# Optimization experiments

Measured on AMD Instinct MI355X. Metric: run time of the kernel, lower is better.

Reference implementation:

```python
import jax, jax.numpy as jnp
import numpy as np

VOCAB = 50257
N_EMBD = 640
BLOCK = 256
B = 16


def setup_inputs() -> dict:
    key = jax.random.key(0)
    ks = jax.random.split(key, 8)
    std = 0.02
    return {
        "idx": jax.random.randint(ks[0], (B, BLOCK), 0, VOCAB, dtype=jnp.int64 if jax.config.jax_enable_x64 else jnp.int32),
        "w_embed": jax.random.normal(ks[1], (VOCAB, N_EMBD), jnp.float32) * std,
        "w_pos": jax.random.normal(ks[2], (BLOCK, N_EMBD), jnp.float32) * std,
        "wq": jax.random.normal(ks[3], (N_EMBD, N_EMBD), jnp.float32) * std,
        "wk": jax.random.normal(ks[4], (N_EMBD, N_EMBD), jnp.float32) * std,
        "wv": jax.random.normal(ks[5], (N_EMBD, N_EMBD), jnp.float32) * std,
        "w_out": jax.random.normal(ks[6], (VOCAB, N_EMBD), jnp.float32) * std,
        "b_out": jnp.zeros((VOCAB,), jnp.float32),
    }


def reference(idx, w_embed, w_pos, wq, wk, wv, w_out, b_out):
    # idx: (B, T) token ids. Dropout is identity (eval mode).
    Bt, T = idx.shape
    x = w_embed[idx] + w_pos[:T]                      # (B, T, D)
    q = jnp.einsum('btd,ed->bte', x, wq)              # torch Linear: x @ W.T
    k = jnp.einsum('btd,ed->bte', x, wk)
    v = jnp.einsum('btd,ed->bte', x, wv)
    scale = jnp.asarray(N_EMBD ** 0.5, x.dtype)
    scores = jnp.einsum('btd,bsd->bts', q, k) / scale  # (B, T, T)
    causal = jnp.triu(jnp.ones((T, T), bool), k=1)     # True above diagonal
    scores = jnp.where(causal, jnp.asarray(-jnp.inf, scores.dtype), scores)
    attn = jax.nn.softmax(scores, axis=-1)
    attn_out = jnp.einsum('bts,bsd->btd', attn, v)     # (B, T, D)
    logits = jnp.einsum('btd,vd->btv', attn_out, w_out) + b_out  # (B, T, V)
    return logits
```

## Files before the change

kernel.cpp:

```cpp
#include <hip/hip_runtime.h>
#include <hip/hip_bf16.h>
#include <stdint.h>

#define VOCAB 50257
#define VPAD  50432
#define DIM   640
#define SEQ   256
#define NBATCH 16
#define MROWS 4096

using bf16 = __hip_bfloat16;
typedef __attribute__((ext_vector_type(8))) short short8;
typedef __attribute__((ext_vector_type(4))) float f32x4;
struct bf16x4 { bf16 a, b, c, d; };

__device__ __forceinline__ void gld_lds16(const void* g, void* l) {
  __builtin_amdgcn_global_load_lds(
      (const __attribute__((address_space(1))) void*)g,
      (__attribute__((address_space(3))) void*)l, 16, 0, 0);
}

#define BAR() asm volatile("s_barrier" ::: "memory")
#define VMC0() asm volatile("s_waitcnt vmcnt(0)" ::: "memory")

__global__ void embed_kernel(const int* __restrict__ idx,
                             const float* __restrict__ we,
                             const float* __restrict__ wp,
                             bf16* __restrict__ xb) {
  int row = blockIdx.x;
  int t = row & (SEQ - 1);
  int tok = idx[row];
  const float* src = we + (long)tok * DIM;
  const float* pos = wp + (long)t * DIM;
  for (int d = threadIdx.x * 4; d < DIM; d += blockDim.x * 4) {
    float4 s = *(const float4*)(src + d);
    float4 p = *(const float4*)(pos + d);
    bf16x4 o = { __float2bfloat16(s.x + p.x), __float2bfloat16(s.y + p.y),
                 __float2bfloat16(s.z + p.z), __float2bfloat16(s.w + p.w) };
    *(bf16x4*)(xb + (long)row * DIM + d) = o;
  }
}

__global__ void conv4_kernel(const float* __restrict__ src, bf16* __restrict__ dst,
                             long n_src, long n_dst) {
  long i = ((long)blockIdx.x * blockDim.x + threadIdx.x) * 4;
  long stride = (long)gridDim.x * blockDim.x * 4;
  for (; i < n_dst; i += stride) {
    float4 v = (i < n_src) ? *(const float4*)(src + i) : make_float4(0.f, 0.f, 0.f, 0.f);
    bf16x4 o = { __float2bfloat16(v.x), __float2bfloat16(v.y),
                 __float2bfloat16(v.z), __float2bfloat16(v.w) };
    *(bf16x4*)(dst + i) = o;
  }
}

__global__ void softmax_kernel(const float* __restrict__ sc, bf16* __restrict__ p) {
  int wid = threadIdx.x >> 6, lane = threadIdx.x & 63;
  int row = blockIdx.x * 4 + wid;
  int t = row & (SEQ - 1);
  const float* srow = sc + (long)row * SEQ;
  const float rsc = 0.03952847075210474f;
  float v[4];
  float mx = -1e30f;
#pragma unroll
  for (int i = 0; i < 4; ++i) {
    int s = lane + 64 * i;
    v[i] = (s <= t) ? srow[s] * rsc : -1e30f;
    mx = fmaxf(mx, v[i]);
  }
#pragma unroll
  for (int off = 32; off; off >>= 1) mx = fmaxf(mx, __shfl_xor(mx, off, 64));
  float sum = 0.f;
#pragma unroll
  for (int i = 0; i < 4; ++i) {
    int s = lane + 64 * i;
    v[i] = (s <= t) ? __expf(v[i] - mx) : 0.f;
    sum += v[i];
  }
#pragma unroll
  for (int off = 32; off; off >>= 1) sum += __shfl_xor(sum, off, 64);
  float inv = 1.f / sum;
#pragma unroll
  for (int i = 0; i < 4; ++i)
    p[(long)row * SEQ + lane + 64 * i] = __float2bfloat16(v[i] * inv);
}

template <int NT, typename OUT_T, bool BIAS, bool TRV>
__global__ __launch_bounds__(256, 4) void gemm_pipe(
    const bf16* __restrict__ Ag, const bf16* __restrict__ Bg,
    OUT_T* __restrict__ Cg, const float* __restrict__ bias,
    int K, int ldc, int Nstore, long sA, long sB, long sC) {
  __shared__ __align__(16) char lds[32768];
  const int tid = threadIdx.x;
  const int lane = tid & 63, wv = tid >> 6;
  const int lr = lane & 15, h16 = lane >> 4;

  const int tm = blockIdx.x, tn = blockIdx.y, bz = blockIdx.z;
  const bf16* A = Ag + (long)bz * sA + (long)tm * 128 * K;
  const bf16* B = Bg + (long)bz * sB + (long)tn * 128 * K;

  int srcE[2], dstW[2];
#pragma unroll
  for (int j = 0; j < 2; ++j) {
    int d = j * 256 + tid;
    int b = d ^ ((d >> 3) & 3);
    srcE[j] = (b >> 2) * K + (b & 3) * 8;
    dstW[j] = (j * 256 + wv * 64) * 16;
  }
  const bf16* aS0 = A + srcE[0];
  const bf16* aS1 = A + srcE[1];
  const bf16* bS0 = B + srcE[0];
  const bf16* bS1 = B + srcE[1];
  auto STAGE = [&](int slot, int t) {
    int kOff = t * 32;
    gld_lds16(aS0 + kOff, lds + slot + dstW[0]);
    gld_lds16(aS1 + kOff, lds + slot + dstW[1]);
    gld_lds16(bS0 + kOff, lds + slot + 8192 + dstW[0]);
    gld_lds16(bS1 + kOff, lds + slot + 8192 + dstW[1]);
  };

  const int wr = (wv >> 1) * 64, wc = (wv & 1) * 64;
  int aoff[4], boff[4];
#pragma unroll
  for (int m = 0; m < 4; ++m) {
    int La = (wr + m * 16 + lr) * 64 + h16 * 16;
    aoff[m] = La ^ (((La >> 7) & 3) << 4);
    int Lb = (wc + m * 16 + lr) * 64 + h16 * 16;
    boff[m] = 8192 + (Lb ^ (((Lb >> 7) & 3) << 4));
  }

  f32x4 acc[4][4] = {};
  short8 a[4], b[4];

  STAGE(0, 0);
  VMC0();
  BAR();

#pragma unroll 2
  for (int t = 0; t < NT; ++t) {
    const int cur = (t & 1) * 16384;
    if (t + 1 < NT) STAGE(16384 - cur, t + 1);
#pragma unroll
    for (int m = 0; m < 4; ++m) a[m] = *(const short8*)(lds + cur + aoff[m]);
#pragma unroll
    for (int n = 0; n < 4; ++n) b[n] = *(const short8*)(lds + cur + boff[n]);
    __builtin_amdgcn_s_setprio(1);
#pragma unroll
    for (int m = 0; m < 4; ++m)
#pragma unroll
      for (int n = 0; n < 4; ++n)
        acc[m][n] = __builtin_amdgcn_mfma_f32_16x16x32_bf16(a[m], b[n], acc[m][n], 0, 0, 0);
    __builtin_amdgcn_s_setprio(0);
    if (t + 1 < NT) VMC0();
    BAR();
  }

  if constexpr (sizeof(OUT_T) == 4) {
    float* Cf = (float*)Cg + (long)bz * sC;
    float bv[4];
#pragma unroll
    for (int n = 0; n < 4; ++n) {
      int col = tn * 128 + wc + lr + n * 16;
      bv[n] = (BIAS && col < Nstore) ? bias[col] : 0.f;
    }
    char* reg = lds + wv * 8192;
    const int rowL = lane & 31, cb = lane >> 5;
#pragma unroll
    for (int mm = 0; mm < 2; ++mm) {
#pragma unroll
      for (int mp = 0; mp < 2; ++mp)
#pragma unroll
        for (int n = 0; n < 4; ++n) {
          f32x4 v = acc[mm * 2 + mp][n];
          v[0] += bv[n]; v[1] += bv[n]; v[2] += bv[n]; v[3] += bv[n];
          int col = lr + n * 16;
          int rho = mp * 16 + h16 * 4;
          int w = col * 32 + (rho ^ ((col & 7) << 2));
          *(f32x4*)(reg + w * 4) = v;
        }
      const long rowg = tm * 128 + wr + mm * 32 + rowL;
#pragma unroll
      for (int k = 0; k < 8; ++k) {
        f32x4 o;
#pragma unroll
        for (int c = 0; c < 4; ++c) {
          int col = k * 8 + cb * 4 + c;
          int w = col * 32 + (rowL ^ ((col & 7) << 2));
          o[c] = *(const float*)(reg + w * 4);
        }
        int gcol = tn * 128 + wc + k * 8 + cb * 4;
        float* dst = Cf + rowg * (long)ldc + gcol;
        if (gcol + 3 < Nstore) {
          *(f32x4*)dst = o;
        } else {
#pragma unroll
          for (int c = 0; c < 4; ++c)
            if (gcol + c < Nstore) dst[c] = o[c];
        }
      }
    }
  } else {
    OUT_T* C = Cg + (long)bz * sC;
    const int crow0 = tm * 128 + wr + h16 * 4;
    const int ccol0 = tn * 128 + wc + lr;
#pragma unroll
    for (int m = 0; m < 4; ++m)
#pragma unroll
      for (int n = 0; n < 4; ++n) {
        int col = ccol0 + n * 16;
        if (col < Nstore) {
#pragma unroll
          for (int j = 0; j < 4; ++j) {
            long row = crow0 + m * 16 + j;
            if constexpr (TRV) {
              C[((long)(row >> 8) * DIM + col) * SEQ + (row & 255)] =
                  __float2bfloat16(acc[m][n][j]);
            } else {
              C[row * ldc + col] = __float2bfloat16(acc[m][n][j]);
            }
          }
        }
      }
  }
}

__global__ __launch_bounds__(256, 6) void scores64(
    const bf16* __restrict__ qg, const bf16* __restrict__ kg,
    float* __restrict__ sc) {
  const int tm = blockIdx.x, tn = blockIdx.y, bz = blockIdx.z;
  if (tn > tm) return;
  __shared__ __align__(16) char lds[16384];
  const int tid = threadIdx.x;
  const int lane = tid & 63, wv = tid >> 6;
  const int lr = lane & 15, h16 = lane >> 4;

  const bf16* A = qg + (long)bz * SEQ * DIM + (long)tm * 64 * DIM;
  const bf16* B = kg + (long)bz * SEQ * DIM + (long)tn * 64 * DIM;

  int srcE, dstW;
  {
    int d = tid;
    int b = d ^ ((d >> 3) & 3);
    srcE = (b >> 2) * DIM + (b & 3) * 8;
    dstW = (wv * 64) * 16;
  }
  auto STAGE = [&](int slot, int t) {
    int kOff = t * 32;
    gld_lds16(A + srcE + kOff, lds + slot + dstW);
    gld_lds16(B + srcE + kOff, lds + slot + 4096 + dstW);
  };

  const int wm = wv >> 1, wn = wv & 1;
  int aoff[2], boff[2];
#pragma unroll
  for (int m = 0; m < 2; ++m) {
    int La = (wm * 32 + m * 16 + lr) * 64 + h16 * 16;
    aoff[m] = La ^ (((La >> 7) & 3) << 4);
    int Lb = (wn * 32 + m * 16 + lr) * 64 + h16 * 16;
    boff[m] = 4096 + (Lb ^ (((Lb >> 7) & 3) << 4));
  }

  f32x4 acc[2][2] = {};
  short8 a[2], b[2];

  STAGE(0, 0);
  VMC0();
  BAR();

#pragma unroll 2
  for (int t = 0; t < 20; ++t) {
    const int cur = (t & 1) * 8192;
    if (t + 1 < 20) STAGE(8192 - cur, t + 1);
#pragma unroll
    for (int m = 0; m < 2; ++m) a[m] = *(const short8*)(lds + cur + aoff[m]);
#pragma unroll
    for (int n = 0; n < 2; ++n) b[n] = *(const short8*)(lds + cur + boff[n]);
    __builtin_amdgcn_s_setprio(1);
#pragma unroll
    for (int m = 0; m < 2; ++m)
#pragma unroll
      for (int n = 0; n < 2; ++n)
        acc[m][n] = __builtin_amdgcn_mfma_f32_16x16x32_bf16(a[m], b[n], acc[m][n], 0, 0, 0);
    __builtin_amdgcn_s_setprio(0);
    if (t + 1 < 20) VMC0();
    BAR();
  }

  float* S = sc + (long)bz * SEQ * SEQ;
  const int crow0 = tm * 64 + wm * 32 + h16 * 4;
  const int ccol0 = tn * 64 + wn * 32 + lr;
#pragma unroll
  for (int m = 0; m < 2; ++m)
#pragma unroll
    for (int n = 0; n < 2; ++n)
#pragma unroll
      for (int j = 0; j < 4; ++j)
        S[(long)(crow0 + m * 16 + j) * SEQ + ccol0 + n * 16] = acc[m][n][j];
}

__global__ __launch_bounds__(512, 6) void gemm8(
    const bf16* __restrict__ Ag, const bf16* __restrict__ Bg,
    float* __restrict__ Cg, const float* __restrict__ bias) {
  __shared__ __align__(16) char lds[32768];
  const int tid = threadIdx.x;
  const int lane = tid & 63, wv = tid >> 6;
  const int lr = lane & 15, h16 = lane >> 4;

  const int tm = blockIdx.x, tn = blockIdx.y;
  const bf16* A = Ag + (long)tm * 128 * DIM;
  const bf16* B = Bg + (long)tn * 128 * DIM;

  int srcE, dstW;
  {
    int d = tid;
    int b = d ^ ((d >> 3) & 3);
    srcE = (b >> 2) * DIM + (b & 3) * 8;
    dstW = (wv * 64) * 16;
  }
  const bf16* aS = A + srcE;
  const bf16* bS = B + srcE;
  auto STAGE = [&](int slot, int t) {
    int kOff = t * 32;
    gld_lds16(aS + kOff, lds + slot + dstW);
    gld_lds16(bS + kOff, lds + slot + 8192 + dstW);
  };

  const int wr = (wv >> 2) * 64, wc = (wv & 3) * 32;
  int aoff[4], boff[2];
#pragma unroll
  for (int m = 0; m < 4; ++m) {
    int La = (wr + m * 16 + lr) * 64 + h16 * 16;
    aoff[m] = La ^ (((La >> 7) & 3) << 4);
  }
#pragma unroll
  for (int n = 0; n < 2; ++n) {
    int Lb = (wc + n * 16 + lr) * 64 + h16 * 16;
    boff[n] = 8192 + (Lb ^ (((Lb >> 7) & 3) << 4));
  }

  f32x4 acc[4][2] = {};
  short8 a[4], b[2];

  STAGE(0, 0);
  VMC0();
  BAR();

#pragma unroll 2
  for (int t = 0; t < 20; ++t) {
    const int cur = (t & 1) * 16384;
    if (t + 1 < 20) STAGE(16384 - cur, t + 1);
#pragma unroll
    for (int m = 0; m < 4; ++m) a[m] = *(const short8*)(lds + cur + aoff[m]);
#pragma unroll
    for (int n = 0; n < 2; ++n) b[n] = *(const short8*)(lds + cur + boff[n]);
    __builtin_amdgcn_s_setprio(1);
#pragma unroll
    for (int m = 0; m < 4; ++m)
#pragma unroll
      for (int n = 0; n < 2; ++n)
        acc[m][n] = __builtin_amdgcn_mfma_f32_16x16x32_bf16(a[m], b[n], acc[m][n], 0, 0, 0);
    __builtin_amdgcn_s_setprio(0);
    if (t + 1 < 20) VMC0();
    BAR();
  }

  const int crow0 = tm * 128 + wr + h16 * 4;
  const int ccol0 = tn * 128 + wc + lr;
  float bv[2];
#pragma unroll
  for (int n = 0; n < 2; ++n) {
    int col = ccol0 + n * 16;
    bv[n] = (col < VOCAB) ? bias[col] : 0.f;
  }
#pragma unroll
  for (int m = 0; m < 4; ++m)
#pragma unroll
    for (int n = 0; n < 2; ++n) {
      int col = ccol0 + n * 16;
      if (col < VOCAB) {
#pragma unroll
        for (int j = 0; j < 4; ++j)
          Cg[(long)(crow0 + m * 16 + j) * VOCAB + col] = acc[m][n][j] + bv[n];
      }
    }
}

extern "C" void kernel_launch(void* const* d_in, const int* in_sizes, int n_in,
                              void* d_out, int out_size, void* d_ws, size_t ws_size,
                              hipStream_t stream) {
  const int*   idx     = (const int*)d_in[0];
  const float* w_embed = (const float*)d_in[1];
  const float* w_pos   = (const float*)d_in[2];
  const float* wq      = (const float*)d_in[3];
  const float* wk      = (const float*)d_in[4];
  const float* wv      = (const float*)d_in[5];
  const float* w_out   = (const float*)d_in[6];
  const float* b_out   = (const float*)d_in[7];
  float* out = (float*)d_out;

  size_t off = 0;
  auto alloc = [&](size_t bytes) {
    void* p = (char*)d_ws + off;
    off += (bytes + 255) & ~(size_t)255;
    return p;
  };
  bf16* x_bf    = (bf16*)alloc((size_t)MROWS * DIM * 2);
  bf16* wqkv_bf = (bf16*)alloc((size_t)3 * DIM * DIM * 2);
  bf16* wout_bf = (bf16*)alloc((size_t)VPAD * DIM * 2);
  bf16* qkv     = (bf16*)alloc((size_t)2 * MROWS * DIM * 2);
  bf16* vT      = (bf16*)alloc((size_t)NBATCH * DIM * SEQ * 2);
  float* scores = (float*)alloc((size_t)NBATCH * SEQ * SEQ * 4);
  bf16* P       = (bf16*)alloc((size_t)NBATCH * SEQ * SEQ * 2);
  bf16* attn    = (bf16*)alloc((size_t)MROWS * DIM * 2);

  const long QKV_S = (long)MROWS * DIM;
  const long W_S   = (long)DIM * DIM;

  embed_kernel<<<MROWS, 256, 0, stream>>>(idx, w_embed, w_pos, x_bf);

  conv4_kernel<<<256, 256, 0, stream>>>(wq, wqkv_bf,           W_S, W_S);
  conv4_kernel<<<256, 256, 0, stream>>>(wk, wqkv_bf + W_S,     W_S, W_S);
  conv4_kernel<<<256, 256, 0, stream>>>(wv, wqkv_bf + 2 * W_S, W_S, W_S);
  conv4_kernel<<<2048, 256, 0, stream>>>(w_out, wout_bf, (long)VOCAB * DIM, (long)VPAD * DIM);

  gemm_pipe<20, bf16, false, false><<<dim3(MROWS / 128, DIM / 128, 2), 256, 0, stream>>>(
      x_bf, wqkv_bf, qkv, nullptr, DIM, DIM, DIM, 0, W_S, QKV_S);

  gemm_pipe<20, bf16, false, true><<<dim3(MROWS / 128, DIM / 128, 1), 256, 0, stream>>>(
      x_bf, wqkv_bf + 2 * W_S, vT, nullptr, DIM, DIM, DIM, 0, 0, 0);

  scores64<<<dim3(4, 4, NBATCH), 256, 0, stream>>>(qkv, qkv + QKV_S, scores);

  softmax_kernel<<<MROWS / 4, 256, 0, stream>>>(scores, P);

  gemm_pipe<8, bf16, false, false><<<dim3(SEQ / 128, DIM / 128, NBATCH), 256, 0, stream>>>(
      P, vT, attn, nullptr, SEQ, DIM, DIM,
      (long)SEQ * SEQ, (long)DIM * SEQ, (long)SEQ * DIM);

  gemm8<<<dim3(MROWS / 128, VPAD / 128), 512, 0, stream>>>(attn, wout_bf, out, b_out);
}
```

Before: 600.2 us.

## Fuse w_out fp32-to-bf16 conversion into output GEMM and merge QKV weight conversions

```diff
diff --git a/kernel.cpp b/kernel.cpp
--- a/kernel.cpp
+++ b/kernel.cpp
@@ -18,6 +18,11 @@
   __builtin_amdgcn_global_load_lds(
       (const __attribute__((address_space(1))) void*)g,
       (__attribute__((address_space(3))) void*)l, 16, 0, 0);
+}
+
+__device__ __forceinline__ short f2bs(float f) {
+  bf16 t = __float2bfloat16(f);
+  return *reinterpret_cast<short*>(&t);
 }
 
 #define BAR() asm volatile("s_barrier" ::: "memory")
@@ -41,15 +46,18 @@
   }
 }
 
-__global__ void conv4_kernel(const float* __restrict__ src, bf16* __restrict__ dst,
-                             long n_src, long n_dst) {
+__global__ void conv3_kernel(const float* __restrict__ s0, const float* __restrict__ s1,
+                             const float* __restrict__ s2, bf16* __restrict__ dst,
+                             long n_each) {
+  const float* src = (blockIdx.y == 0) ? s0 : (blockIdx.y == 1) ? s1 : s2;
+  bf16* d = dst + (long)blockIdx.y * n_each;
   long i = ((long)blockIdx.x * blockDim.x + threadIdx.x) * 4;
   long stride = (long)gridDim.x * blockDim.x * 4;
-  for (; i < n_dst; i += stride) {
-    float4 v = (i < n_src) ? *(const float4*)(src + i) : make_float4(0.f, 0.f, 0.f, 0.f);
+  for (; i < n_each; i += stride) {
+    float4 v = *(const float4*)(src + i);
     bf16x4 o = { __float2bfloat16(v.x), __float2bfloat16(v.y),
                  __float2bfloat16(v.z), __float2bfloat16(v.w) };
-    *(bf16x4*)(dst + i) = o;
+    *(bf16x4*)(d + i) = o;
   }
 }
 
@@ -297,35 +305,45 @@
         S[(long)(crow0 + m * 16 + j) * SEQ + ccol0 + n * 16] = acc[m][n][j];
 }
 
-__global__ __launch_bounds__(512, 6) void gemm8(
-    const bf16* __restrict__ Ag, const bf16* __restrict__ Bg,
+__global__ __launch_bounds__(512, 6) void gemm8f(
+    const bf16* __restrict__ Ag, const float* __restrict__ Wg,
     float* __restrict__ Cg, const float* __restrict__ bias) {
-  __shared__ __align__(16) char lds[32768];
+  __shared__ __align__(16) char lds[49152];
   const int tid = threadIdx.x;
   const int lane = tid & 63, wv = tid >> 6;
   const int lr = lane & 15, h16 = lane >> 4;
 
   const int tm = blockIdx.x, tn = blockIdx.y;
   const bf16* A = Ag + (long)tm * 128 * DIM;
-  const bf16* B = Bg + (long)tn * 128 * DIM;
-
-  int srcE, dstW;
+
+  const bf16* aS;
+  int dstA;
   {
     int d = tid;
     int b = d ^ ((d >> 3) & 3);
-    srcE = (b >> 2) * DIM + (b & 3) * 8;
-    dstW = (wv * 64) * 16;
-  }
-  const bf16* aS = A + srcE;
-  const bf16* bS = B + srcE;
+    aS = A + (b >> 2) * DIM + (b & 3) * 8;
+    dstA = (wv * 64) * 16;
+  }
+  const float* bS[2];
+  int dstB[2];
+#pragma unroll
+  for (int j = 0; j < 2; ++j) {
+    int d = j * 512 + tid;
+    int b = d ^ ((d >> 3) & 7);
+    int grow = tn * 128 + (b >> 3);
+    if (grow > VOCAB - 1) grow = VOCAB - 1;
+    bS[j] = Wg + (long)grow * DIM + (b & 7) * 4;
+    dstB[j] = 8192 + (j * 512 + wv * 64) * 16;
+  }
   auto STAGE = [&](int slot, int t) {
-    int kOff = t * 32;
-    gld_lds16(aS + kOff, lds + slot + dstW);
-    gld_lds16(bS + kOff, lds + slot + 8192 + dstW);
+    gld_lds16(aS + t * 32, lds + slot + dstA);
+#pragma unroll
+    for (int j = 0; j < 2; ++j)
+      gld_lds16(bS[j] + t * 32, lds + slot + dstB[j]);
   };
 
   const int wr = (wv >> 2) * 64, wc = (wv & 3) * 32;
-  int aoff[4], boff[2];
+  int aoff[4], boff[2][2];
 #pragma unroll
   for (int m = 0; m < 4; ++m) {
     int La = (wr + m * 16 + lr) * 64 + h16 * 16;
@@ -333,8 +351,10 @@
   }
 #pragma unroll
   for (int n = 0; n < 2; ++n) {
-    int Lb = (wc + n * 16 + lr) * 64 + h16 * 16;
-    boff[n] = 8192 + (Lb ^ (((Lb >> 7) & 3) << 4));
+    int L = (wc + n * 16 + lr) * 128 + h16 * 32;
+    boff[n][0] = 8192 + (L ^ (((L >> 7) & 7) << 4));
+    int L1 = L + 16;
+    boff[n][1] = 8192 + (L1 ^ (((L1 >> 7) & 7) << 4));
   }
 
   f32x4 acc[4][2] = {};
@@ -346,12 +366,19 @@
 
 #pragma unroll 2
   for (int t = 0; t < 20; ++t) {
-    const int cur = (t & 1) * 16384;
-    if (t + 1 < 20) STAGE(16384 - cur, t + 1);
+    const int cur = (t & 1) * 24576;
+    if (t + 1 < 20) STAGE(24576 - cur, t + 1);
 #pragma unroll
     for (int m = 0; m < 4; ++m) a[m] = *(const short8*)(lds + cur + aoff[m]);
 #pragma unroll
-    for (int n = 0; n < 2; ++n) b[n] = *(const short8*)(lds + cur + boff[n]);
+    for (int n = 0; n < 2; ++n) {
+      f32x4 lo = *(const f32x4*)(lds + cur + boff[n][0]);
+      f32x4 hi = *(const f32x4*)(lds + cur + boff[n][1]);
+      short8 bb;
+      bb[0] = f2bs(lo[0]); bb[1] = f2bs(lo[1]); bb[2] = f2bs(lo[2]); bb[3] = f2bs(lo[3]);
+      bb[4] = f2bs(hi[0]); bb[5] = f2bs(hi[1]); bb[6] = f2bs(hi[2]); bb[7] = f2bs(hi[3]);
+      b[n] = bb;
+    }
     __builtin_amdgcn_s_setprio(1);
 #pragma unroll
     for (int m = 0; m < 4; ++m)
@@ -405,7 +432,6 @@
   };
   bf16* x_bf    = (bf16*)alloc((size_t)MROWS * DIM * 2);
   bf16* wqkv_bf = (bf16*)alloc((size_t)3 * DIM * DIM * 2);
-  bf16* wout_bf = (bf16*)alloc((size_t)VPAD * DIM * 2);
   bf16* qkv     = (bf16*)alloc((size_t)2 * MROWS * DIM * 2);
   bf16* vT      = (bf16*)alloc((size_t)NBATCH * DIM * SEQ * 2);
   float* scores = (float*)alloc((size_t)NBATCH * SEQ * SEQ * 4);
@@ -417,10 +443,7 @@
 
   embed_kernel<<<MROWS, 256, 0, stream>>>(idx, w_embed, w_pos, x_bf);
 
-  conv4_kernel<<<256, 256, 0, stream>>>(wq, wqkv_bf,           W_S, W_S);
-  conv4_kernel<<<256, 256, 0, stream>>>(wk, wqkv_bf + W_S,     W_S, W_S);
-  conv4_kernel<<<256, 256, 0, stream>>>(wv, wqkv_bf + 2 * W_S, W_S, W_S);
-  conv4_kernel<<<2048, 256, 0, stream>>>(w_out, wout_bf, (long)VOCAB * DIM, (long)VPAD * DIM);
+  conv3_kernel<<<dim3(256, 3), 256, 0, stream>>>(wq, wk, wv, wqkv_bf, W_S);
 
   gemm_pipe<20, bf16, false, false><<<dim3(MROWS / 128, DIM / 128, 2), 256, 0, stream>>>(
       x_bf, wqkv_bf, qkv, nullptr, DIM, DIM, DIM, 0, W_S, QKV_S);
@@ -436,5 +459,5 @@
       P, vT, attn, nullptr, SEQ, DIM, DIM,
       (long)SEQ * SEQ, (long)DIM * SEQ, (long)SEQ * DIM);
 
-  gemm8<<<dim3(MROWS / 128, VPAD / 128), 512, 0, stream>>>(attn, wout_bf, out, b_out);
-}
+  gemm8f<<<dim3(MROWS / 128, VPAD / 128), 512, 0, stream>>>(attn, w_out, out, b_out);
+}
```

After: 757.4 us. +26.2%, slower.

## Replace output GEMM with 256x256-tile persistent-column kernel and deeper pipelining

Applied to the files above, without the earlier changes.

```diff
diff --git a/kernel.cpp b/kernel.cpp
--- a/kernel.cpp
+++ b/kernel.cpp
@@ -3,7 +3,7 @@
 #include <stdint.h>
 
 #define VOCAB 50257
-#define VPAD  50432
+#define VPAD3 51200
 #define DIM   640
 #define SEQ   256
 #define NBATCH 16
@@ -21,6 +21,7 @@
 }
 
 #define BAR() asm volatile("s_barrier" ::: "memory")
+#define VMC(n) asm volatile("s_waitcnt vmcnt(" #n ")" ::: "memory")
 #define VMC0() asm volatile("s_waitcnt vmcnt(0)" ::: "memory")
 
 __global__ void embed_kernel(const int* __restrict__ idx,
@@ -297,91 +298,133 @@
         S[(long)(crow0 + m * 16 + j) * SEQ + ccol0 + n * 16] = acc[m][n][j];
 }
 
-__global__ __launch_bounds__(512, 6) void gemm8(
+__global__ __launch_bounds__(512, 1) void gemm256m(
     const bf16* __restrict__ Ag, const bf16* __restrict__ Bg,
     float* __restrict__ Cg, const float* __restrict__ bias) {
-  __shared__ __align__(16) char lds[32768];
+  __shared__ __align__(16) char lds[131072];
   const int tid = threadIdx.x;
   const int lane = tid & 63, wv = tid >> 6;
+  const int wm = wv >> 2, wn = wv & 3;
+  const int tm = blockIdx.x;
+  const int tg = blockIdx.y;
+
+  int e0, e1, du0, du1;
+  {
+    int L0 = tid * 16;
+    int L1 = (512 + tid) * 16;
+    int Lp0 = L0 ^ (((L0 >> 9) & 1) << 5);
+    int Lp1 = L1 ^ (((L1 >> 9) & 1) << 5);
+    e0 = ((Lp0 >> 6) & 127) * DIM + ((Lp0 >> 13) & 1) * 32 + ((Lp0 & 63) >> 1);
+    e1 = ((Lp1 >> 6) & 127) * DIM + ((Lp1 >> 13) & 1) * 32 + ((Lp1 & 63) >> 1);
+    du0 = (wv << 6) * 16;
+    du1 = (512 + (wv << 6)) * 16;
+  }
+  auto STAGE = [&](int halfBase, const bf16* src) {
+    gld_lds16(src + e0, lds + halfBase + du0);
+    gld_lds16(src + e1, lds + halfBase + du1);
+  };
+
+  const bf16* Ab = Ag + (long)tm * 256 * DIM;
+  const long STRIDE = (long)256 * DIM;
+
   const int lr = lane & 15, h16 = lane >> 4;
-
-  const int tm = blockIdx.x, tn = blockIdx.y;
-  const bf16* A = Ag + (long)tm * 128 * DIM;
-  const bf16* B = Bg + (long)tn * 128 * DIM;
-
-  int srcE, dstW;
-  {
-    int d = tid;
-    int b = d ^ ((d >> 3) & 3);
-    srcE = (b >> 2) * DIM + (b & 3) * 8;
-    dstW = (wv * 64) * 16;
-  }
-  const bf16* aS = A + srcE;
-  const bf16* bS = B + srcE;
-  auto STAGE = [&](int slot, int t) {
-    int kOff = t * 32;
-    gld_lds16(aS + kOff, lds + slot + dstW);
-    gld_lds16(bS + kOff, lds + slot + 8192 + dstW);
-  };
-
-  const int wr = (wv >> 2) * 64, wc = (wv & 3) * 32;
-  int aoff[4], boff[2];
-#pragma unroll
-  for (int m = 0; m < 4; ++m) {
-    int La = (wr + m * 16 + lr) * 64 + h16 * 16;
-    aoff[m] = La ^ (((La >> 7) & 3) << 4);
-  }
-#pragma unroll
-  for (int n = 0; n < 2; ++n) {
-    int Lb = (wc + n * 16 + lr) * 64 + h16 * 16;
-    boff[n] = 8192 + (Lb ^ (((Lb >> 7) & 3) << 4));
-  }
-
-  f32x4 acc[4][2] = {};
-  short8 a[4], b[2];
-
-  STAGE(0, 0);
-  VMC0();
+  const int laneOff = (lr * 64 + h16 * 16) ^ ((lr & 8) << 2);
+  const int abase = wm * 16384 + laneOff;
+  const int bbase = 32768 + (wn >> 1) * 16384 + (wn & 1) * 4096 + laneOff;
+
+  f32x4 acc[8][4] = {};
+  short8 a0[2][4], a1[2][4], b[2][4];
+
+#define READ_A(DST, SLOT, MFB)                                                \
+  { _Pragma("unroll") for (int ks = 0; ks < 2; ++ks)                          \
+    _Pragma("unroll") for (int mf = 0; mf < 4; ++mf)                          \
+      DST[ks][mf] = *(const short8*)(lds + (SLOT) + abase + ks * 8192 +       \
+                                     ((MFB) + mf) * 1024); }
+#define READ_B(SLOT)                                                          \
+  { _Pragma("unroll") for (int ks = 0; ks < 2; ++ks)                          \
+    _Pragma("unroll") for (int nf = 0; nf < 4; ++nf)                          \
+      b[ks][nf] = *(const short8*)(lds + (SLOT) + bbase + ks * 8192 +         \
+                                   nf * 1024); }
+#define MFMA_G(AARR, KS, ROFF)                                                \
+  __builtin_amdgcn_s_setprio(1);                                              \
+  { _Pragma("unroll") for (int mf = 0; mf < 4; ++mf)                          \
+    _Pragma("unroll") for (int nf = 0; nf < 4; ++nf)                          \
+      acc[(ROFF) + mf][nf] = __builtin_amdgcn_mfma_f32_16x16x32_bf16(         \
+          AARR[KS][mf], b[KS][nf], acc[(ROFF) + mf][nf], 0, 0, 0); }          \
+  __builtin_amdgcn_s_setprio(0);
+
+  const bf16* Bc = Bg + (long)tg * 4 * STRIDE;
+
+  STAGE(0,             Ab);
+  STAGE(16384,         Ab + 128 * DIM);
+  STAGE(32768,         Bc);
+  STAGE(49152,         Bc + 128 * DIM);
+  STAGE(65536 + 32768, Bc + 64);
+  STAGE(65536 + 0,     Ab + 64);
+  STAGE(65536 + 16384, Ab + 128 * DIM + 64);
+  VMC(6);
   BAR();
 
-#pragma unroll 2
-  for (int t = 0; t < 20; ++t) {
-    const int cur = (t & 1) * 16384;
-    if (t + 1 < 20) STAGE(16384 - cur, t + 1);
-#pragma unroll
-    for (int m = 0; m < 4; ++m) a[m] = *(const short8*)(lds + cur + aoff[m]);
-#pragma unroll
-    for (int n = 0; n < 2; ++n) b[n] = *(const short8*)(lds + cur + boff[n]);
-    __builtin_amdgcn_s_setprio(1);
-#pragma unroll
-    for (int m = 0; m < 4; ++m)
-#pragma unroll
-      for (int n = 0; n < 2; ++n)
-        acc[m][n] = __builtin_amdgcn_mfma_f32_16x16x32_bf16(a[m], b[n], acc[m][n], 0, 0, 0);
-    __builtin_amdgcn_s_setprio(0);
-    if (t + 1 < 20) VMC0();
-    BAR();
-  }
-
-  const int crow0 = tm * 128 + wr + h16 * 4;
-  const int ccol0 = tn * 128 + wc + lr;
-  float bv[2];
-#pragma unroll
-  for (int n = 0; n < 2; ++n) {
-    int col = ccol0 + n * 16;
-    bv[n] = (col < VOCAB) ? bias[col] : 0.f;
-  }
-#pragma unroll
-  for (int m = 0; m < 4; ++m)
-#pragma unroll
-    for (int n = 0; n < 2; ++n) {
-      int col = ccol0 + n * 16;
-      if (col < VOCAB) {
-#pragma unroll
-        for (int j = 0; j < 4; ++j)
-          Cg[(long)(crow0 + m * 16 + j) * VOCAB + col] = acc[m][n][j] + bv[n];
+  for (int s = 0; s < 4; ++s) {
+    const bf16* Bn = Bc + STRIDE;
+    const bool sNotLast = (s < 3);
+#pragma unroll
+    for (int T = 0; T < 10; ++T) {
+      const int slot = (T & 1) << 16;
+      const int nslot = ((T + 1) & 1) << 16;
+      const int k1 = (T < 9) ? (T + 1) * 64 : 0;
+      const int k2 = (T < 8) ? (T + 2) * 64 : (T - 8) * 64;
+      const bf16* B1src = (T < 9) ? Bc : Bn;
+      const bf16* B2src = (T < 8) ? Bc : Bn;
+      const bool ok1 = sNotLast || (T < 9);
+      const bool ok2 = sNotLast || (T < 8);
+      READ_A(a0, slot, 0);
+      READ_B(slot);
+      if (ok1) STAGE(nslot + 49152, B1src + 128 * DIM + k1);
+      BAR();
+      MFMA_G(a0, 0, 0);
+      BAR();
+      READ_A(a1, slot, 4);
+      if (ok2) STAGE(slot + 32768, B2src + k2);
+      BAR();
+      MFMA_G(a0, 1, 0);
+      BAR();
+      if (ok2) STAGE(slot + 0, Ab + k2);
+      BAR();
+      MFMA_G(a1, 0, 4);
+      BAR();
+      if (ok2) {
+        STAGE(slot + 16384, Ab + 128 * DIM + k2);
+        VMC(6);
+      } else if (ok1) {
+        VMC(0);
       }
+      BAR();
+      MFMA_G(a1, 1, 4);
+      BAR();
     }
+    {
+      const int rowB = tm * 256 + wm * 128 + h16 * 4;
+      const int colB = (tg * 4 + s) * 256 + wn * 64 + lr;
+#pragma unroll
+      for (int mf = 0; mf < 8; ++mf)
+#pragma unroll
+        for (int nf = 0; nf < 4; ++nf) {
+          int col = colB + nf * 16;
+          if (col < VOCAB) {
+            float bv = bias[col];
+#pragma unroll
+            for (int jj = 0; jj < 4; ++jj)
+              Cg[(long)(rowB + mf * 16 + jj) * VOCAB + col] = acc[mf][nf][jj] + bv;
+          }
+          acc[mf][nf] = (f32x4){0.f, 0.f, 0.f, 0.f};
+        }
+    }
+    Bc = Bn;
+  }
+#undef READ_A
+#undef READ_B
+#undef MFMA_G
 }
 
 extern "C" void kernel_launch(void* const* d_in, const int* in_sizes, int n_in,
@@ -405,7 +448,7 @@
   };
   bf16* x_bf    = (bf16*)alloc((size_t)MROWS * DIM * 2);
   bf16* wqkv_bf = (bf16*)alloc((size_t)3 * DIM * DIM * 2);
-  bf16* wout_bf = (bf16*)alloc((size_t)VPAD * DIM * 2);
+  bf16* wout_bf = (bf16*)alloc((size_t)VPAD3 * DIM * 2);
   bf16* qkv     = (bf16*)alloc((size_t)2 * MROWS * DIM * 2);
   bf16* vT      = (bf16*)alloc((size_t)NBATCH * DIM * SEQ * 2);
   float* scores = (float*)alloc((size_t)NBATCH * SEQ * SEQ * 4);
@@ -420,7 +463,7 @@
   conv4_kernel<<<256, 256, 0, stream>>>(wq, wqkv_bf,           W_S, W_S);
   conv4_kernel<<<256, 256, 0, stream>>>(wk, wqkv_bf + W_S,     W_S, W_S);
   conv4_kernel<<<256, 256, 0, stream>>>(wv, wqkv_bf + 2 * W_S, W_S, W_S);
-  conv4_kernel<<<2048, 256, 0, stream>>>(w_out, wout_bf, (long)VOCAB * DIM, (long)VPAD * DIM);
+  conv4_kernel<<<2048, 256, 0, stream>>>(w_out, wout_bf, (long)VOCAB * DIM, (long)VPAD3 * DIM);
 
   gemm_pipe<20, bf16, false, false><<<dim3(MROWS / 128, DIM / 128, 2), 256, 0, stream>>>(
       x_bf, wqkv_bf, qkv, nullptr, DIM, DIM, DIM, 0, W_S, QKV_S);
@@ -436,5 +479,5 @@
       P, vT, attn, nullptr, SEQ, DIM, DIM,
       (long)SEQ * SEQ, (long)DIM * SEQ, (long)SEQ * DIM);
 
-  gemm8<<<dim3(MROWS / 128, VPAD / 128), 512, 0, stream>>>(attn, wout_bf, out, b_out);
-}
+  gemm256m<<<dim3(MROWS / 256, VPAD3 / 1024), 512, 0, stream>>>(attn, wout_bf, out, b_out);
+}
```

After: 1.019 ms. +69.7%, slower.
